# Performance work log

Measured on AMD Instinct MI355X. Metric: run time of the kernel, lower is better.

The kernel has to match this reference:

```python
import jax, jax.numpy as jnp
import numpy as np

N = 10000
E = 320000
F_IN = 256
F_PROJ = 200


def setup_inputs() -> dict:
    key = jax.random.key(0)
    ks = jax.random.split(key, 8)
    x = jax.random.normal(ks[0], (N, F_IN), dtype=jnp.float32)
    edge_attr = jax.random.uniform(ks[1], (N, N), dtype=jnp.float32)
    src = jax.random.randint(ks[2], (E,), 0, N)
    dst = jax.random.randint(ks[3], (E,), 0, N)
    # remove self loops at data-gen time (module calls remove_self_loops)
    dst = jnp.where(dst == src, (dst + 1) % N, dst)
    edge_index = jnp.stack([src, dst]).astype(jnp.int64)
    W_proj = jax.random.normal(ks[4], (F_IN, F_PROJ), dtype=jnp.float32) * 0.05
    b_proj = jnp.zeros((F_PROJ,), dtype=jnp.float32)
    W_att = jax.random.normal(ks[5], (F_PROJ, 1), dtype=jnp.float32) * 0.05
    b_att = jnp.zeros((1,), dtype=jnp.float32)
    return {"x": x, "edge_attr": edge_attr, "edge_index": edge_index,
            "W_proj": W_proj, "b_proj": b_proj, "W_att": W_att, "b_att": b_att}


def reference(x, edge_attr, edge_index, W_proj, b_proj, W_att, b_att):
    src, dst = edge_index[0], edge_index[1]
    # gather: x_j = source features, x_i = target features (PyG default flow)
    x_i = x[dst]                      # [E, F_IN]
    x_j = x[src]                      # [E, F_IN]
    p_i = x_i @ W_proj + b_proj       # [E, 200]
    p_j = x_j @ W_proj + b_proj       # [E, 200]
    alpha = jnp.abs(p_i - p_j) @ W_att + b_att   # [E, 1]
    alpha = jax.nn.relu(alpha)
    alpha = jax.nn.softmax(alpha, axis=0)        # softmax over edges
    a = alpha[:, 0]
    # write attention symmetrically into the dense edge matrix
    edge_values = edge_attr.at[src, dst].set(a).at[dst, src].set(a)
    # scatter-max aggregation of (unprojected) x_i by target index
    agg = jax.ops.segment_max(x_i, dst, num_segments=N)
    agg = jnp.where(jnp.isfinite(agg), agg, jnp.zeros((), agg.dtype))
    return agg, edge_values
```

## Files before the change

kernel.cpp:

```cpp
#include <hip/hip_runtime.h>

#define N_NODES 10000
#define E_EDGES 320000
#define F_IN    256
#define F_PROJ  200

#define ALPHA_BLOCKS 2048
#define COPY_BLOCKS  4096
#define FUSED_BLOCKS (ALPHA_BLOCKS + COPY_BLOCKS)
#define ALPHA_WAVES  (ALPHA_BLOCKS * 4)
#define ALPHA_CHUNK  ((E_EDGES + ALPHA_WAVES - 1) / ALPHA_WAVES)

typedef float vfloat4 __attribute__((ext_vector_type(4)));

__device__ __forceinline__ unsigned short f32_to_bf16(float f) {
    unsigned int u = __float_as_uint(f);
    u += 0x7FFFu + ((u >> 16) & 1u);
    return (unsigned short)(u >> 16);
}
__device__ __forceinline__ float bf16_to_f32(unsigned short b) {
    return __uint_as_float(((unsigned int)b) << 16);
}

__global__ void proj_kernel(const float* __restrict__ x,
                            const float* __restrict__ W,
                            unsigned short* __restrict__ P,
                            int* __restrict__ flags,
                            float* __restrict__ sumbuf) {
    int gt = blockIdx.x * 256 + threadIdx.x;
    if (gt < N_NODES) flags[gt] = 0;
    if (gt == N_NODES) *sumbuf = 0.f;

    __shared__ float xs[8][F_IN];
    int n0 = blockIdx.x * 8;
    for (int i = threadIdx.x; i < 8 * F_IN; i += 256) {
        int r = i >> 8, c = i & 255;
        xs[r][c] = x[(n0 + r) * F_IN + c];
    }
    __syncthreads();
    int j = threadIdx.x;
    if (j >= F_PROJ) return;
    float acc[8] = {0.f,0.f,0.f,0.f,0.f,0.f,0.f,0.f};
    for (int k = 0; k < F_IN; ++k) {
        float w = W[k * F_PROJ + j];
        #pragma unroll
        for (int r = 0; r < 8; ++r) acc[r] += xs[r][k] * w;
    }
    #pragma unroll
    for (int r = 0; r < 8; ++r) P[(long)(n0 + r) * F_PROJ + j] = f32_to_bf16(acc[r]);
}

__global__ __launch_bounds__(256) void alpha_copy_kernel(
                             const int* __restrict__ ei,
                             const unsigned short* __restrict__ P,
                             const float* __restrict__ Watt,
                             const float* __restrict__ batt,
                             float* __restrict__ expalpha,
                             float* __restrict__ sumbuf,
                             int* __restrict__ flags,
                             const vfloat4* __restrict__ csrc,
                             vfloat4* __restrict__ cdst,
                             long n4) {
    int role = blockIdx.x % 3;
    if (role != 0) {
        long cid = (long)(blockIdx.x / 3) * 2 + (role - 1);
        long i = cid * 256 + threadIdx.x;
        const long stride = (long)COPY_BLOCKS * 256;
        while (i + stride < n4) {
            vfloat4 v0 = __builtin_nontemporal_load(csrc + i);
            vfloat4 v1 = __builtin_nontemporal_load(csrc + i + stride);
            __builtin_nontemporal_store(v0, cdst + i);
            __builtin_nontemporal_store(v1, cdst + i + stride);
            i += 2 * stride;
        }
        if (i < n4) {
            vfloat4 v = __builtin_nontemporal_load(csrc + i);
            __builtin_nontemporal_store(v, cdst + i);
        }
        return;
    }
    __shared__ float bsum;
    if (threadIdx.x == 0) bsum = 0.f;
    __syncthreads();

    int aid  = blockIdx.x / 3;
    int wid  = aid * 4 + (threadIdx.x >> 6);
    int lane = threadIdx.x & 63;

    float4 w4 = make_float4(0.f, 0.f, 0.f, 0.f);
    if (lane < 50) w4 = ((const float4*)Watt)[lane];
    float bias = batt[0];

    int e0 = wid * ALPHA_CHUNK;
    int e1 = min(e0 + ALPHA_CHUNK, E_EDGES);
    float lsum = 0.f;

    for (int e = e0; e < e1; ++e) {
        int s = ei[e];
        int d = ei[E_EDGES + e];
        float acc = 0.f;
        if (lane < 50) {
            uint2 us = *(const uint2*)(P + (long)s * F_PROJ + lane * 4);
            uint2 ud = *(const uint2*)(P + (long)d * F_PROJ + lane * 4);
            float s0 = bf16_to_f32((unsigned short)(us.x & 0xFFFF));
            float s1 = bf16_to_f32((unsigned short)(us.x >> 16));
            float s2 = bf16_to_f32((unsigned short)(us.y & 0xFFFF));
            float s3 = bf16_to_f32((unsigned short)(us.y >> 16));
            float d0 = bf16_to_f32((unsigned short)(ud.x & 0xFFFF));
            float d1 = bf16_to_f32((unsigned short)(ud.x >> 16));
            float d2 = bf16_to_f32((unsigned short)(ud.y & 0xFFFF));
            float d3 = bf16_to_f32((unsigned short)(ud.y >> 16));
            acc = fabsf(d0 - s0) * w4.x + fabsf(d1 - s1) * w4.y
                + fabsf(d2 - s2) * w4.z + fabsf(d3 - s3) * w4.w;
        }
        #pragma unroll
        for (int off = 32; off; off >>= 1) acc += __shfl_down(acc, off);
        if (lane == 0) {
            float alpha = fmaxf(acc + bias, 0.f);
            float ea = expf(alpha);
            expalpha[e] = ea;
            flags[d] = 1;
            lsum += ea;
        }
    }
    if (lane == 0) atomicAdd(&bsum, lsum);
    __syncthreads();
    if (threadIdx.x == 0) atomicAdd(sumbuf, bsum);
}

__global__ void scatter_agg_kernel(const int* __restrict__ ei,
                                   const float* __restrict__ expalpha,
                                   const float* __restrict__ sumbuf,
                                   float* __restrict__ ev,
                                   const float4* __restrict__ x4,
                                   const int* __restrict__ flags,
                                   float4* __restrict__ agg4) {
    int b = blockIdx.x;
    if (b < 2500) {
        int i4 = b * 256 + threadIdx.x;
        float4 v = x4[i4];
        if (!flags[i4 >> 6]) v = make_float4(0.f, 0.f, 0.f, 0.f);
        agg4[i4] = v;
    } else {
        int e = (b - 2500) * 256 + threadIdx.x;
        if (e >= E_EDGES) return;
        float a = expalpha[e] / sumbuf[0];
        int s = ei[e];
        int d = ei[E_EDGES + e];
        ev[(long)s * N_NODES + d] = a;
        ev[(long)d * N_NODES + s] = a;
    }
}

extern "C" void kernel_launch(void* const* d_in, const int* in_sizes, int n_in,
                              void* d_out, int out_size, void* d_ws, size_t ws_size,
                              hipStream_t stream) {
    (void)in_sizes; (void)n_in; (void)out_size; (void)ws_size;
    const float* x         = (const float*)d_in[0];
    const float* edge_attr = (const float*)d_in[1];
    const int*   ei        = (const int*)d_in[2];
    const float* W_proj    = (const float*)d_in[3];
    const float* W_att     = (const float*)d_in[5];
    const float* b_att     = (const float*)d_in[6];

    float* agg = (float*)d_out;
    float* ev  = (float*)d_out + (long)N_NODES * F_IN;

    char* ws = (char*)d_ws;
    unsigned short* P = (unsigned short*)(ws);
    float* expalpha   = (float*)(ws + 4000000);
    float* sumbuf     = (float*)(ws + 5280000);
    int*   flags      = (int*)  (ws + 5280016);

    proj_kernel<<<N_NODES / 8, 256, 0, stream>>>(x, W_proj, P, flags, sumbuf);

    long n4 = (long)N_NODES * N_NODES / 4;
    alpha_copy_kernel<<<FUSED_BLOCKS, 256, 0, stream>>>(
        ei, P, W_att, b_att, expalpha, sumbuf, flags,
        (const vfloat4*)edge_attr, (vfloat4*)ev, n4);

    scatter_agg_kernel<<<2500 + (E_EDGES + 255) / 256, 256, 0, stream>>>(
        ei, expalpha, sumbuf, ev, (const float4*)x, flags, (float4*)agg);
}
```

Before: 251.6 us.

## Overlap edge_attr copy with projection and move agg into alpha kernel

The dense 400MB edge_attr copy is split so part of it runs alongside the projection kernel and the rest alongside the alpha computation, using a 1:3 alpha-to-copy block ratio. Flag setting moves into the projection kernel, and the masked agg copy moves into the alpha blocks, which leaves the final kernel as a pure scatter. Flags and the sum are now zeroed by a memset instead of inside a kernel. This hides more of the projection latency under bandwidth-bound copying, at the cost of an extra memset launch and fewer alpha waves.

```diff
diff --git a/kernel.cpp b/kernel.cpp
--- a/kernel.cpp
+++ b/kernel.cpp
@@ -5,11 +5,20 @@
 #define F_IN    256
 #define F_PROJ  200
 
-#define ALPHA_BLOCKS 2048
-#define COPY_BLOCKS  4096
-#define FUSED_BLOCKS (ALPHA_BLOCKS + COPY_BLOCKS)
-#define ALPHA_WAVES  (ALPHA_BLOCKS * 4)
-#define ALPHA_CHUNK  ((E_EDGES + ALPHA_WAVES - 1) / ALPHA_WAVES)
+#define N4_TOTAL 25000000L
+#define S1_SPLIT 4000000L
+
+#define K1_PROJ_BLOCKS 1250
+#define K1_COPY_BLOCKS 768
+#define K1_BLOCKS (K1_PROJ_BLOCKS + K1_COPY_BLOCKS)
+
+#define K2_BLOCKS 6144
+#define K2_ALPHA_BLOCKS 1536
+#define K2_COPY_BLOCKS (K2_BLOCKS - K2_ALPHA_BLOCKS)
+#define K2_ALPHA_WAVES (K2_ALPHA_BLOCKS * 4)
+#define ALPHA_CHUNK ((E_EDGES + K2_ALPHA_WAVES - 1) / K2_ALPHA_WAVES)
+#define AGG_N4 (N_NODES * F_IN / 4)
+#define AGG_CHUNK ((AGG_N4 + K2_ALPHA_BLOCKS - 1) / K2_ALPHA_BLOCKS)
 
 typedef float vfloat4 __attribute__((ext_vector_type(4)));
 
@@ -22,23 +31,40 @@
     return __uint_as_float(((unsigned int)b) << 16);
 }
 
-__global__ void proj_kernel(const float* __restrict__ x,
-                            const float* __restrict__ W,
-                            unsigned short* __restrict__ P,
-                            int* __restrict__ flags,
-                            float* __restrict__ sumbuf) {
-    int gt = blockIdx.x * 256 + threadIdx.x;
-    if (gt < N_NODES) flags[gt] = 0;
-    if (gt == N_NODES) *sumbuf = 0.f;
+__global__ __launch_bounds__(256) void k1_proj_flags_copy(
+        const float* __restrict__ x,
+        const float* __restrict__ W,
+        unsigned short* __restrict__ P,
+        const int* __restrict__ ei,
+        int* __restrict__ flags,
+        const vfloat4* __restrict__ csrc,
+        vfloat4* __restrict__ cdst) {
+    int bid = blockIdx.x, tid = threadIdx.x;
+    if (bid >= K1_PROJ_BLOCKS) {
+        long i = (long)(bid - K1_PROJ_BLOCKS) * 256 + tid;
+        const long stride = (long)K1_COPY_BLOCKS * 256;
+        while (i + stride < S1_SPLIT) {
+            vfloat4 v0 = __builtin_nontemporal_load(csrc + i);
+            vfloat4 v1 = __builtin_nontemporal_load(csrc + i + stride);
+            __builtin_nontemporal_store(v0, cdst + i);
+            __builtin_nontemporal_store(v1, cdst + i + stride);
+            i += 2 * stride;
+        }
+        if (i < S1_SPLIT) {
+            vfloat4 v = __builtin_nontemporal_load(csrc + i);
+            __builtin_nontemporal_store(v, cdst + i);
+        }
+        return;
+    }
+    int gt = bid * 256 + tid;
+    flags[ei[E_EDGES + gt]] = 1;
 
     __shared__ float xs[8][F_IN];
-    int n0 = blockIdx.x * 8;
-    for (int i = threadIdx.x; i < 8 * F_IN; i += 256) {
-        int r = i >> 8, c = i & 255;
-        xs[r][c] = x[(n0 + r) * F_IN + c];
-    }
+    int n0 = bid * 8;
+    for (int i = tid; i < 8 * F_IN / 4; i += 256)
+        ((float4*)xs)[i] = ((const float4*)(x + (long)n0 * F_IN))[i];
     __syncthreads();
-    int j = threadIdx.x;
+    int j = tid;
     if (j >= F_PROJ) return;
     float acc[8] = {0.f,0.f,0.f,0.f,0.f,0.f,0.f,0.f};
     for (int k = 0; k < F_IN; ++k) {
@@ -50,42 +76,44 @@
     for (int r = 0; r < 8; ++r) P[(long)(n0 + r) * F_PROJ + j] = f32_to_bf16(acc[r]);
 }
 
-__global__ __launch_bounds__(256) void alpha_copy_kernel(
-                             const int* __restrict__ ei,
-                             const unsigned short* __restrict__ P,
-                             const float* __restrict__ Watt,
-                             const float* __restrict__ batt,
-                             float* __restrict__ expalpha,
-                             float* __restrict__ sumbuf,
-                             int* __restrict__ flags,
-                             const vfloat4* __restrict__ csrc,
-                             vfloat4* __restrict__ cdst,
-                             long n4) {
-    int role = blockIdx.x % 3;
+__global__ __launch_bounds__(256) void k2_alpha_agg_copy(
+        const int* __restrict__ ei,
+        const unsigned short* __restrict__ P,
+        const float* __restrict__ Watt,
+        const float* __restrict__ batt,
+        float* __restrict__ expalpha,
+        float* __restrict__ sumbuf,
+        const int* __restrict__ flags,
+        const float4* __restrict__ x4,
+        float4* __restrict__ agg4,
+        const vfloat4* __restrict__ csrc,
+        vfloat4* __restrict__ cdst) {
+    int bid = blockIdx.x, tid = threadIdx.x;
+    int role = bid & 3;
     if (role != 0) {
-        long cid = (long)(blockIdx.x / 3) * 2 + (role - 1);
-        long i = cid * 256 + threadIdx.x;
-        const long stride = (long)COPY_BLOCKS * 256;
-        while (i + stride < n4) {
+        long cid = (long)(bid >> 2) * 3 + (role - 1);
+        long i = S1_SPLIT + cid * 256 + tid;
+        const long stride = (long)K2_COPY_BLOCKS * 256;
+        while (i + stride < N4_TOTAL) {
             vfloat4 v0 = __builtin_nontemporal_load(csrc + i);
             vfloat4 v1 = __builtin_nontemporal_load(csrc + i + stride);
             __builtin_nontemporal_store(v0, cdst + i);
             __builtin_nontemporal_store(v1, cdst + i + stride);
             i += 2 * stride;
         }
-        if (i < n4) {
+        if (i < N4_TOTAL) {
             vfloat4 v = __builtin_nontemporal_load(csrc + i);
             __builtin_nontemporal_store(v, cdst + i);
         }
         return;
     }
     __shared__ float bsum;
-    if (threadIdx.x == 0) bsum = 0.f;
+    if (tid == 0) bsum = 0.f;
     __syncthreads();
 
-    int aid  = blockIdx.x / 3;
-    int wid  = aid * 4 + (threadIdx.x >> 6);
-    int lane = threadIdx.x & 63;
+    int aid  = bid >> 2;
+    int wid  = aid * 4 + (tid >> 6);
+    int lane = tid & 63;
 
     float4 w4 = make_float4(0.f, 0.f, 0.f, 0.f);
     if (lane < 50) w4 = ((const float4*)Watt)[lane];
@@ -102,16 +130,14 @@
         if (lane < 50) {
             uint2 us = *(const uint2*)(P + (long)s * F_PROJ + lane * 4);
             uint2 ud = *(const uint2*)(P + (long)d * F_PROJ + lane * 4);
-            float s0 = bf16_to_f32((unsigned short)(us.x & 0xFFFF));
-            float s1 = bf16_to_f32((unsigned short)(us.x >> 16));
-            float s2 = bf16_to_f32((unsigned short)(us.y & 0xFFFF));
-            float s3 = bf16_to_f32((unsigned short)(us.y >> 16));
-            float d0 = bf16_to_f32((unsigned short)(ud.x & 0xFFFF));
-            float d1 = bf16_to_f32((unsigned short)(ud.x >> 16));
-            float d2 = bf16_to_f32((unsigned short)(ud.y & 0xFFFF));
-            float d3 = bf16_to_f32((unsigned short)(ud.y >> 16));
-            acc = fabsf(d0 - s0) * w4.x + fabsf(d1 - s1) * w4.y
-                + fabsf(d2 - s2) * w4.z + fabsf(d3 - s3) * w4.w;
+            acc = fabsf(bf16_to_f32((unsigned short)(ud.x & 0xFFFF)) -
+                        bf16_to_f32((unsigned short)(us.x & 0xFFFF))) * w4.x
+                + fabsf(bf16_to_f32((unsigned short)(ud.x >> 16)) -
+                        bf16_to_f32((unsigned short)(us.x >> 16))) * w4.y
+                + fabsf(bf16_to_f32((unsigned short)(ud.y & 0xFFFF)) -
+                        bf16_to_f32((unsigned short)(us.y & 0xFFFF))) * w4.z
+                + fabsf(bf16_to_f32((unsigned short)(ud.y >> 16)) -
+                        bf16_to_f32((unsigned short)(us.y >> 16))) * w4.w;
         }
         #pragma unroll
         for (int off = 32; off; off >>= 1) acc += __shfl_down(acc, off);
@@ -119,37 +145,34 @@
             float alpha = fmaxf(acc + bias, 0.f);
             float ea = expf(alpha);
             expalpha[e] = ea;
-            flags[d] = 1;
             lsum += ea;
         }
     }
     if (lane == 0) atomicAdd(&bsum, lsum);
     __syncthreads();
-    if (threadIdx.x == 0) atomicAdd(sumbuf, bsum);
-}
-
-__global__ void scatter_agg_kernel(const int* __restrict__ ei,
-                                   const float* __restrict__ expalpha,
-                                   const float* __restrict__ sumbuf,
-                                   float* __restrict__ ev,
-                                   const float4* __restrict__ x4,
-                                   const int* __restrict__ flags,
-                                   float4* __restrict__ agg4) {
-    int b = blockIdx.x;
-    if (b < 2500) {
-        int i4 = b * 256 + threadIdx.x;
-        float4 v = x4[i4];
-        if (!flags[i4 >> 6]) v = make_float4(0.f, 0.f, 0.f, 0.f);
-        agg4[i4] = v;
-    } else {
-        int e = (b - 2500) * 256 + threadIdx.x;
-        if (e >= E_EDGES) return;
-        float a = expalpha[e] / sumbuf[0];
-        int s = ei[e];
-        int d = ei[E_EDGES + e];
-        ev[(long)s * N_NODES + d] = a;
-        ev[(long)d * N_NODES + s] = a;
-    }
+    if (tid == 0) atomicAdd(sumbuf, bsum);
+
+    long a0 = (long)aid * AGG_CHUNK;
+    long a1 = a0 + AGG_CHUNK; if (a1 > AGG_N4) a1 = AGG_N4;
+    for (long i = a0 + tid; i < a1; i += 256) {
+        float4 v = x4[i];
+        if (!flags[i >> 6]) v = make_float4(0.f, 0.f, 0.f, 0.f);
+        agg4[i] = v;
+    }
+}
+
+__global__ __launch_bounds__(256) void k3_scatter(
+        const int* __restrict__ ei,
+        const float* __restrict__ expalpha,
+        const float* __restrict__ sumbuf,
+        float* __restrict__ ev) {
+    int e = blockIdx.x * 256 + threadIdx.x;
+    if (e >= E_EDGES) return;
+    float a = expalpha[e] / sumbuf[0];
+    int s = ei[e];
+    int d = ei[E_EDGES + e];
+    ev[(long)s * N_NODES + d] = a;
+    ev[(long)d * N_NODES + s] = a;
 }
 
 extern "C" void kernel_launch(void* const* d_in, const int* in_sizes, int n_in,
@@ -169,16 +192,18 @@
     char* ws = (char*)d_ws;
     unsigned short* P = (unsigned short*)(ws);
     float* expalpha   = (float*)(ws + 4000000);
-    float* sumbuf     = (float*)(ws + 5280000);
-    int*   flags      = (int*)  (ws + 5280016);
-
-    proj_kernel<<<N_NODES / 8, 256, 0, stream>>>(x, W_proj, P, flags, sumbuf);
-
-    long n4 = (long)N_NODES * N_NODES / 4;
-    alpha_copy_kernel<<<FUSED_BLOCKS, 256, 0, stream>>>(
+    int*   flags      = (int*)  (ws + 5280000);
+    float* sumbuf     = (float*)(ws + 5320000);
+
+    hipMemsetAsync(ws + 5280000, 0, 40016, stream);
+
+    k1_proj_flags_copy<<<K1_BLOCKS, 256, 0, stream>>>(
+        x, W_proj, P, ei, flags, (const vfloat4*)edge_attr, (vfloat4*)ev);
+
+    k2_alpha_agg_copy<<<K2_BLOCKS, 256, 0, stream>>>(
         ei, P, W_att, b_att, expalpha, sumbuf, flags,
-        (const vfloat4*)edge_attr, (vfloat4*)ev, n4);
-
-    scatter_agg_kernel<<<2500 + (E_EDGES + 255) / 256, 256, 0, stream>>>(
-        ei, expalpha, sumbuf, ev, (const float4*)x, flags, (float4*)agg);
-}
+        (const float4*)x, (float4*)agg,
+        (const vfloat4*)edge_attr, (vfloat4*)ev);
+
+    k3_scatter<<<(E_EDGES + 255) / 256, 256, 0, stream>>>(ei, expalpha, sumbuf, ev);
+}
```

Result: no change. 249.3 us (-0.9%).
